# Kernel tuning notes

Hardware: AMD Instinct MI355X
Metric: run time of the kernel (lower is better)

Reference implementation:

```python
import jax, jax.numpy as jnp
import numpy as np

DN = ('NHWC', 'HWIO', 'NHWC')

def _conv(x, w, b, pad):
    y = jax.lax.conv_general_dilated(x, w, (1, 1), pad, dimension_numbers=DN)
    return y + b

def setup_inputs() -> dict:
    key = jax.random.key(0)
    ks = jax.random.split(key, 8)
    C = 256  # FPN channels
    sizes = [256, 128, 64, 32, 16]  # P2..P6 for 1024x1024 input
    d = {}
    for i, s in enumerate(sizes):
        d[f'p{i + 2}'] = jax.random.normal(ks[i], (2, s, s, C), jnp.float32)
    d['w_share'] = jax.random.normal(ks[5], (3, 3, C, 512), jnp.float32) * 0.02
    d['b_share'] = jnp.zeros((512,), jnp.float32)
    d['w_cls'] = jax.random.normal(ks[6], (1, 1, 512, 6), jnp.float32) * 0.02
    d['b_cls'] = jnp.zeros((6,), jnp.float32)
    d['w_box'] = jax.random.normal(ks[7], (1, 1, 512, 12), jnp.float32) * 0.02
    d['b_box'] = jnp.zeros((12,), jnp.float32)
    return d

def reference(p2, p3, p4, p5, p6, w_share, b_share, w_cls, b_cls, w_box, b_box):
    logits, probs, boxes = [], [], []
    for f in (p2, p3, p4, p5, p6):  # fixed small loop over pyramid levels
        s = jax.nn.relu(_conv(f, w_share, b_share, 'SAME'))
        cl = _conv(s, w_cls, b_cls, 'VALID')
        B = cl.shape[0]
        cl = cl.reshape(B, -1, 2)  # (B, H*W*3, 2)
        cp = jax.nn.softmax(cl, axis=-1)
        bp = _conv(s, w_box, b_box, 'VALID').reshape(B, -1, 4)  # (B, H*W*3, 4)
        logits.append(cl)
        probs.append(cp)
        boxes.append(bp)
    class_logit = jnp.concatenate(logits, axis=1)
    class_prob = jnp.concatenate(probs, axis=1)
    box_pred = jnp.concatenate(boxes, axis=1)
    return (class_logit, class_prob, box_pred)
```

## Files before the change

kernel.cpp:

```cpp
#include <hip/hip_runtime.h>
#include <hip/hip_bf16.h>


typedef __attribute__((ext_vector_type(8))) short short8;
typedef __attribute__((ext_vector_type(4))) float f32x4;

#define HALO_B 23040
#define LDS_BYTES 131072

static __device__ __forceinline__ unsigned short f2bf(float f) {
    unsigned u = __float_as_uint(f);
    u += 0x7fffu + ((u >> 16) & 1u);
    return (unsigned short)(u >> 16);
}

__global__ void prep_wt(const float* __restrict__ w, unsigned short* __restrict__ wt) {
    int t = blockIdx.x * 256 + threadIdx.x;
    if (t >= 147456) return;
    int co = t & 511;
    int k0 = (t >> 9) << 3;
    short8 v;
#pragma unroll
    for (int j = 0; j < 8; ++j)
        v[j] = (short)f2bf(w[(size_t)(k0 + j) * 512 + co]);
    *(short8*)(wt + (size_t)co * 2304 + k0) = v;
}

__global__ void prep_whead(const float* __restrict__ wc, const float* __restrict__ wb,
                           unsigned short* __restrict__ wh) {
    int t = blockIdx.x * 256 + threadIdx.x;
    if (t >= 16384) return;
    int j = t >> 9, k = t & 511;
    float v = 0.f;
    if (j < 6) v = wc[k * 6 + j];
    else if (j < 18) v = wb[k * 12 + (j - 6)];
    wh[t] = f2bf(v);
}

__global__ __launch_bounds__(512) void rpn_main(
    const float* __restrict__ p2, const float* __restrict__ p3,
    const float* __restrict__ p4, const float* __restrict__ p5,
    const float* __restrict__ p6,
    const unsigned short* __restrict__ wt, const unsigned short* __restrict__ wh,
    const float* __restrict__ bsh, const float* __restrict__ bcl,
    const float* __restrict__ bbx, float* __restrict__ out) {
    extern __shared__ char smem[];
    const int tid = threadIdx.x;
    const int lane = tid & 63, wid = tid >> 6;

    int b = blockIdx.x, lvl, rem;
    if (b < 1024)      { lvl = 0; rem = b; }
    else if (b < 1280) { lvl = 1; rem = b - 1024; }
    else if (b < 1344) { lvl = 2; rem = b - 1280; }
    else if (b < 1360) { lvl = 3; rem = b - 1344; }
    else               { lvl = 4; rem = b - 1360; }
    const int Hs[5]   = {256, 128, 64, 32, 16};
    const int LOFF[5] = {0, 196608, 245760, 258048, 261120};
    const int H = Hs[lvl];
    const int lvloff = LOFF[lvl];
    const float* inp = lvl == 0 ? p2 : lvl == 1 ? p3 : lvl == 2 ? p4 : lvl == 3 ? p5 : p6;
    const int tilesX = H >> 4;
    const int tilesPerImg = (H >> 3) * tilesX;
    const int n = rem / tilesPerImg;
    const int tt = rem % tilesPerImg;
    const int y0 = (tt / tilesX) << 3;
    const int x0 = (tt % tilesX) << 4;
    const float* inb = inp + (size_t)n * H * H * 256;

    f32x4 acc[8][4];
    const f32x4 zero4 = {0.f, 0.f, 0.f, 0.f};
#pragma unroll
    for (int i = 0; i < 8; ++i)
#pragma unroll
        for (int j = 0; j < 4; ++j) acc[i][j] = zero4;

    float sv[3][8];
    int saddr[3];

    auto stage_load = [&](int cc) {
#pragma unroll
        for (int i = 0; i < 3; ++i) {
            int u = tid + (i << 9);
            saddr[i] = -1;
            if (u < 1440) {
                int ch8 = u & 7;
                int rc = u >> 3;
                int col = rc % 18;
                int row = rc / 18;
                int y = y0 + row - 1, x = x0 + col - 1;
                saddr[i] = rc * 128 + ((ch8 * 16) ^ ((col & 7) << 4));
                if (y >= 0 && y < H && x >= 0 && x < H) {
                    const float* src = inb + (size_t)(y * H + x) * 256 + cc * 64 + ch8 * 8;
                    float4 a = *(const float4*)(src);
                    float4 c = *(const float4*)(src + 4);
                    sv[i][0] = a.x; sv[i][1] = a.y; sv[i][2] = a.z; sv[i][3] = a.w;
                    sv[i][4] = c.x; sv[i][5] = c.y; sv[i][6] = c.z; sv[i][7] = c.w;
                } else {
#pragma unroll
                    for (int j = 0; j < 8; ++j) sv[i][j] = 0.f;
                }
            }
        }
    };
    auto stage_write = [&](char* buf) {
#pragma unroll
        for (int i = 0; i < 3; ++i) {
            if (saddr[i] >= 0) {
                short8 v;
#pragma unroll
                for (int j = 0; j < 8; ++j) v[j] = (short)f2bf(sv[i][j]);
                *(short8*)(buf + saddr[i]) = v;
            }
        }
    };

    stage_load(0);
    stage_write(smem);
    __syncthreads();

    for (int cc = 0; cc < 4; ++cc) {
        if (cc < 3) stage_load(cc + 1);
        const char* hb = smem + (cc & 1) * HALO_B;
#pragma unroll
        for (int ty = 0; ty < 3; ++ty) {
#pragma unroll
            for (int tx = 0; tx < 3; ++tx) {
#pragma unroll
                for (int kk = 0; kk < 2; ++kk) {
                    const int hc = (lane & 15) + tx;
                    const int chb = (kk * 32 + ((lane >> 4) << 3)) * 2;
                    const int sw = (hc & 7) << 4;
                    short8 af[8];
#pragma unroll
                    for (int mi = 0; mi < 8; ++mi) {
                        int hr = mi + ty;
                        af[mi] = *(const short8*)(hb + (hr * 18 + hc) * 128 + (chb ^ sw));
                    }
                    const int kof = (ty * 3 + tx) * 256 + cc * 64 + kk * 32 + ((lane >> 4) << 3);
                    short8 bf[4];
#pragma unroll
                    for (int ni = 0; ni < 4; ++ni) {
                        int co = wid * 64 + ni * 16 + (lane & 15);
                        bf[ni] = *(const short8*)(wt + (size_t)co * 2304 + kof);
                    }
#pragma unroll
                    for (int mi = 0; mi < 8; ++mi)
#pragma unroll
                        for (int ni = 0; ni < 4; ++ni)
                            acc[mi][ni] = __builtin_amdgcn_mfma_f32_16x16x32_bf16(
                                af[mi], bf[ni], acc[mi][ni], 0, 0, 0);
                }
            }
        }
        if (cc < 3) stage_write(smem + ((cc + 1) & 1) * HALO_B);
        __syncthreads();
    }

#pragma unroll
    for (int ni = 0; ni < 4; ++ni) {
        int co = wid * 64 + ni * 16 + (lane & 15);
        float bias = bsh[co];
#pragma unroll
        for (int mi = 0; mi < 8; ++mi) {
#pragma unroll
            for (int r = 0; r < 4; ++r) {
                int p = mi * 16 + ((lane >> 4) << 2) + r;
                float v = fmaxf(acc[mi][ni][r] + bias, 0.f);
                int addr = (p * 1024 + co * 2) ^ ((p & 7) << 4);
                *(unsigned short*)(smem + addr) = f2bf(v);
            }
        }
    }
    __syncthreads();

    f32x4 h0 = zero4, h1 = zero4;
    {
        const int prow = (wid << 4) + (lane & 15);
        const int swz = (prow & 7) << 4;
        const int kbase = (lane >> 4) << 3;
#pragma unroll
        for (int kk = 0; kk < 16; ++kk) {
            int k = (kk << 5) + kbase;
            short8 a = *(const short8*)(smem + ((prow * 1024 + k * 2) ^ swz));
            short8 b0 = *(const short8*)(wh + (lane & 15) * 512 + k);
            short8 b1 = *(const short8*)(wh + (16 + (lane & 15)) * 512 + k);
            h0 = __builtin_amdgcn_mfma_f32_16x16x32_bf16(a, b0, h0, 0, 0, 0);
            h1 = __builtin_amdgcn_mfma_f32_16x16x32_bf16(a, b1, h1, 0, 0, 0);
        }
    }

    const int jj = lane & 15;
    float bh0;
    if (jj < 6) bh0 = bcl[jj]; else bh0 = bbx[jj - 6];
    float bh1 = 0.f;
    if (jj < 2) bh1 = bbx[10 + jj];
    const size_t O1 = 1047552, O2 = 2095104;
    const int yg = y0 + wid;
    const size_t nb = (size_t)n * 261888;
#pragma unroll
    for (int r = 0; r < 4; ++r) {
        int c_sp = ((lane >> 4) << 2) + r;
        int xg = x0 + c_sp;
        size_t base3 = (size_t)lvloff + (size_t)(yg * H + xg) * 3;
        float v0 = h0[r] + bh0;
        float po = __shfl_xor(v0, 1, 64);
        if (jj < 6) {
            int a_ = jj >> 1, c_ = jj & 1;
            size_t idx = (nb + base3 + a_) * 2 + c_;
            out[idx] = v0;
            out[O1 + idx] = 1.f / (1.f + expf(po - v0));
        } else {
            int q = jj - 6;
            out[O2 + (nb + base3 + (q >> 2)) * 4 + (q & 3)] = v0;
        }
        if (jj < 2) {
            float v1 = h1[r] + bh1;
            out[O2 + (nb + base3 + 2) * 4 + (2 + jj)] = v1;
        }
    }
}

extern "C" void kernel_launch(void* const* d_in, const int* in_sizes, int n_in,
                              void* d_out, int out_size, void* d_ws, size_t ws_size,
                              hipStream_t stream) {
    const float* p2  = (const float*)d_in[0];
    const float* p3  = (const float*)d_in[1];
    const float* p4  = (const float*)d_in[2];
    const float* p5  = (const float*)d_in[3];
    const float* p6  = (const float*)d_in[4];
    const float* wsh = (const float*)d_in[5];
    const float* bsh = (const float*)d_in[6];
    const float* wcl = (const float*)d_in[7];
    const float* bcl = (const float*)d_in[8];
    const float* wbx = (const float*)d_in[9];
    const float* bbx = (const float*)d_in[10];
    unsigned short* wt = (unsigned short*)d_ws;
    unsigned short* wh = wt + 512 * 2304;
    float* out = (float*)d_out;

    (void)hipFuncSetAttribute((const void*)rpn_main,
                              hipFuncAttributeMaxDynamicSharedMemorySize, LDS_BYTES);
    prep_wt<<<576, 256, 0, stream>>>(wsh, wt);
    prep_whead<<<64, 256, 0, stream>>>(wcl, wbx, wh);
    rpn_main<<<1364, 512, LDS_BYTES, stream>>>(p2, p3, p4, p5, p6, wt, wh,
                                               bsh, bcl, bbx, out);
}
```

Baseline: 1.426 ms.

## Pre-convert inputs to bf16 and stage halos with direct global-to-LDS loads

Adds a separate pass that converts all five pyramid feature maps to bf16 in workspace. The main conv kernel then fills its double-buffered halo tiles with asynchronous global_load_lds 16-byte copies, with the XOR swizzle moved to the source channel index, instead of loading fp32 into registers, converting and writing LDS. LDS is zeroed once up front so out-of-bounds halo slots stay zero. The aim is to shrink the staging instruction count, register pressure and per-tile fp32 traffic, at the cost of an extra full read/write pass over the inputs and a launch_bounds change to one block per CU.

```diff
diff --git a/kernel.cpp b/kernel.cpp
--- a/kernel.cpp
+++ b/kernel.cpp
@@ -12,6 +12,12 @@
     unsigned u = __float_as_uint(f);
     u += 0x7fffu + ((u >> 16) & 1u);
     return (unsigned short)(u >> 16);
+}
+
+static __device__ __forceinline__ void gload_lds16(const void* g, void* l) {
+    __builtin_amdgcn_global_load_lds(
+        (const __attribute__((address_space(1))) unsigned int*)g,
+        (__attribute__((address_space(3))) unsigned int*)l, 16, 0, 0);
 }
 
 __global__ void prep_wt(const float* __restrict__ w, unsigned short* __restrict__ wt) {
@@ -37,10 +43,32 @@
     wh[t] = f2bf(v);
 }
 
-__global__ __launch_bounds__(512) void rpn_main(
-    const float* __restrict__ p2, const float* __restrict__ p3,
-    const float* __restrict__ p4, const float* __restrict__ p5,
-    const float* __restrict__ p6,
+__global__ void prep_bf16(const float* __restrict__ p2, const float* __restrict__ p3,
+                          const float* __restrict__ p4, const float* __restrict__ p5,
+                          const float* __restrict__ p6, unsigned short* __restrict__ xb) {
+    const size_t NU = 5586944;
+    for (size_t u = (size_t)blockIdx.x * blockDim.x + threadIdx.x; u < NU;
+         u += (size_t)gridDim.x * blockDim.x) {
+        size_t e = u << 3;
+        const float* src;
+        if (e < 33554432u)      src = p2 + e;
+        else if (e < 41943040u) src = p3 + (e - 33554432u);
+        else if (e < 44040192u) src = p4 + (e - 41943040u);
+        else if (e < 44564480u) src = p5 + (e - 44040192u);
+        else                    src = p6 + (e - 44564480u);
+        f32x4 a = __builtin_nontemporal_load((const f32x4*)src);
+        f32x4 b = __builtin_nontemporal_load((const f32x4*)src + 1);
+        short8 v;
+        v[0] = (short)f2bf(a[0]); v[1] = (short)f2bf(a[1]);
+        v[2] = (short)f2bf(a[2]); v[3] = (short)f2bf(a[3]);
+        v[4] = (short)f2bf(b[0]); v[5] = (short)f2bf(b[1]);
+        v[6] = (short)f2bf(b[2]); v[7] = (short)f2bf(b[3]);
+        *(short8*)(xb + e) = v;
+    }
+}
+
+__global__ __launch_bounds__(512, 1) void rpn_main(
+    const unsigned short* __restrict__ xb,
     const unsigned short* __restrict__ wt, const unsigned short* __restrict__ wh,
     const float* __restrict__ bsh, const float* __restrict__ bcl,
     const float* __restrict__ bbx, float* __restrict__ out) {
@@ -56,16 +84,26 @@
     else               { lvl = 4; rem = b - 1360; }
     const int Hs[5]   = {256, 128, 64, 32, 16};
     const int LOFF[5] = {0, 196608, 245760, 258048, 261120};
+    const size_t XOFF[5] = {0, 33554432u, 41943040u, 44040192u, 44564480u};
     const int H = Hs[lvl];
     const int lvloff = LOFF[lvl];
-    const float* inp = lvl == 0 ? p2 : lvl == 1 ? p3 : lvl == 2 ? p4 : lvl == 3 ? p5 : p6;
     const int tilesX = H >> 4;
     const int tilesPerImg = (H >> 3) * tilesX;
     const int n = rem / tilesPerImg;
     const int tt = rem % tilesPerImg;
     const int y0 = (tt / tilesX) << 3;
     const int x0 = (tt % tilesX) << 4;
-    const float* inb = inp + (size_t)n * H * H * 256;
+    const unsigned short* inb = xb + XOFF[lvl] + (size_t)n * H * H * 256;
+
+    {
+        const int4 z4 = {0, 0, 0, 0};
+#pragma unroll
+        for (int i = 0; i < 6; ++i) {
+            int s = tid + (i << 9);
+            if (s < 2880) *(int4*)(smem + s * 16) = z4;
+        }
+    }
+    __syncthreads();
 
     f32x4 acc[8][4];
     const f32x4 zero4 = {0.f, 0.f, 0.f, 0.f};
@@ -74,52 +112,29 @@
 #pragma unroll
         for (int j = 0; j < 4; ++j) acc[i][j] = zero4;
 
-    float sv[3][8];
-    int saddr[3];
-
-    auto stage_load = [&](int cc) {
-#pragma unroll
-        for (int i = 0; i < 3; ++i) {
-            int u = tid + (i << 9);
-            saddr[i] = -1;
-            if (u < 1440) {
-                int ch8 = u & 7;
-                int rc = u >> 3;
-                int col = rc % 18;
-                int row = rc / 18;
-                int y = y0 + row - 1, x = x0 + col - 1;
-                saddr[i] = rc * 128 + ((ch8 * 16) ^ ((col & 7) << 4));
-                if (y >= 0 && y < H && x >= 0 && x < H) {
-                    const float* src = inb + (size_t)(y * H + x) * 256 + cc * 64 + ch8 * 8;
-                    float4 a = *(const float4*)(src);
-                    float4 c = *(const float4*)(src + 4);
-                    sv[i][0] = a.x; sv[i][1] = a.y; sv[i][2] = a.z; sv[i][3] = a.w;
-                    sv[i][4] = c.x; sv[i][5] = c.y; sv[i][6] = c.z; sv[i][7] = c.w;
-                } else {
-#pragma unroll
-                    for (int j = 0; j < 8; ++j) sv[i][j] = 0.f;
-                }
+    auto stage = [&](int cc, int bufsel) {
+        char* sbase = smem + bufsel * HALO_B;
+#pragma unroll
+        for (int r = 0; r < 3; ++r) {
+            int u = (r << 9) + tid;
+            int rc = u >> 3, s8 = u & 7;
+            int col = rc % 18, row = rc / 18;
+            int y = y0 + row - 1, x = x0 + col - 1;
+            if (u < 1440 && y >= 0 && y < H && x >= 0 && x < H) {
+                int ch = s8 ^ (col & 7);
+                const unsigned short* src =
+                    inb + (size_t)(y * H + x) * 256 + cc * 64 + ch * 8;
+                char* ldst = sbase + (((r << 9) + (wid << 6)) << 4);
+                gload_lds16(src, ldst);
             }
         }
     };
-    auto stage_write = [&](char* buf) {
-#pragma unroll
-        for (int i = 0; i < 3; ++i) {
-            if (saddr[i] >= 0) {
-                short8 v;
-#pragma unroll
-                for (int j = 0; j < 8; ++j) v[j] = (short)f2bf(sv[i][j]);
-                *(short8*)(buf + saddr[i]) = v;
-            }
-        }
-    };
-
-    stage_load(0);
-    stage_write(smem);
+
+    stage(0, 0);
     __syncthreads();
 
     for (int cc = 0; cc < 4; ++cc) {
-        if (cc < 3) stage_load(cc + 1);
+        if (cc < 3) stage(cc + 1, (cc + 1) & 1);
         const char* hb = smem + (cc & 1) * HALO_B;
 #pragma unroll
         for (int ty = 0; ty < 3; ++ty) {
@@ -152,7 +167,6 @@
                 }
             }
         }
-        if (cc < 3) stage_write(smem + ((cc + 1) & 1) * HALO_B);
         __syncthreads();
     }
 
@@ -235,13 +249,14 @@
     const float* wbx = (const float*)d_in[9];
     const float* bbx = (const float*)d_in[10];
     unsigned short* wt = (unsigned short*)d_ws;
-    unsigned short* wh = wt + 512 * 2304;
+    unsigned short* wh = wt + 1179648;
+    unsigned short* xb = wh + 16384;
     float* out = (float*)d_out;
 
     (void)hipFuncSetAttribute((const void*)rpn_main,
                               hipFuncAttributeMaxDynamicSharedMemorySize, LDS_BYTES);
     prep_wt<<<576, 256, 0, stream>>>(wsh, wt);
     prep_whead<<<64, 256, 0, stream>>>(wcl, wbx, wh);
-    rpn_main<<<1364, 512, LDS_BYTES, stream>>>(p2, p3, p4, p5, p6, wt, wh,
-                                               bsh, bcl, bbx, out);
-}
+    prep_bf16<<<4096, 256, 0, stream>>>(p2, p3, p4, p5, p6, xb);
+    rpn_main<<<1364, 512, LDS_BYTES, stream>>>(xb, wt, wh, bsh, bcl, bbx, out);
+}
```

New measurement: 1.293 ms. 9.4% less time.
